# Kernel optimization log

Hardware: AMD Instinct MI355X
Metric: run time of the kernel (lower is better)

The kernel has to match this reference:

```python
import jax, jax.numpy as jnp
import numpy as np

ATOMS_PER_RES = 24  # hard-coded in .view(B, N_l, -1, 24)
NEG_SLOPE = 0.01    # nn.LeakyReLU default


def setup_inputs() -> dict:
    key = jax.random.key(0)
    ks = jax.random.split(key, 10)
    B, N_l, N_p, H, G = 16, 64, 512, 128, 10
    pos_l = jax.random.normal(ks[0], (B, N_l, 3), jnp.float32) * 5.0
    pos_p = jax.random.normal(ks[1], (B, N_p, ATOMS_PER_RES, 3), jnp.float32) * 5.0
    Interact = jax.random.normal(ks[2], (B, N_l, N_p, H), jnp.float32)
    Interact_mask = jax.random.randint(ks[3], (B, N_l, N_p), 0, 2) > 0
    W_pi = jax.random.normal(ks[4], (H, G), jnp.float32) * 0.05
    b_pi = jnp.zeros((G,), jnp.float32)
    W_sigma = jax.random.normal(ks[5], (H, G), jnp.float32) * 0.05
    b_sigma = jnp.zeros((G,), jnp.float32)
    W_mu = jax.random.normal(ks[6], (H, G), jnp.float32) * 0.05
    b_mu = jnp.zeros((G,), jnp.float32)
    return {
        "pos_l": pos_l, "pos_p": pos_p, "Interact": Interact,
        "Interact_mask": Interact_mask,
        "W_pi": W_pi, "b_pi": b_pi,
        "W_sigma": W_sigma, "b_sigma": b_sigma,
        "W_mu": W_mu, "b_mu": b_mu,
    }


def _min_dist(pos_l, pos_p):
    # pos_l: [B, N_l, 3]; pos_p: [B, N_p, 24, 3]
    B, N_l, _ = pos_l.shape
    Y = pos_p.reshape(B, -1, 3)  # [B, N_p*24, 3]
    d2 = (jnp.sum(pos_l * pos_l, axis=-1)[..., None]
          + jnp.sum(Y * Y, axis=-1)[:, None, :]
          - 2.0 * jnp.einsum('bic,bjc->bij', pos_l, Y))  # [B, N_l, N_p*24]
    dist = jnp.nan_to_num(jnp.sqrt(d2), nan=10000.0)
    # min over the 24 atoms of each residue -> [B, N_l, N_p]
    return dist.reshape(B, N_l, -1, ATOMS_PER_RES).min(axis=-1)


def reference(pos_l, pos_p, Interact, Interact_mask,
              W_pi, b_pi, W_sigma, b_sigma, W_mu, b_mu):
    leaky = lambda x: jax.nn.leaky_relu(x, NEG_SLOPE)
    dist = _min_dist(pos_l, pos_p)                       # [B, N_l, N_p]
    # original gathers dist[Interact_mask]; keep static shape, zero-fill masked-out
    dist_masked = jnp.where(Interact_mask, dist, 0.0)
    pi = jax.nn.softmax(Interact @ W_pi + b_pi, axis=-1)          # [B,N_l,N_p,G]
    sigma = jnp.clip(leaky(Interact @ W_sigma + b_sigma) + 1.1, 1e-6, None)
    mu = leaky(Interact @ W_mu + b_mu) + 1.0
    return pi, sigma, mu, dist_masked, Interact_mask
```

## Files before the change

### kernel.cpp

```cpp
#include <hip/hip_runtime.h>
#include <cmath>

#define NB 16
#define NL 64
#define NP 512
#define NH 128
#define NG 10
#define ROWS (NB * NL * NP)

#define OFF_PI    ((size_t)0)
#define OFF_SIGMA ((size_t)5242880)
#define OFF_MU    ((size_t)10485760)
#define OFF_DIST  ((size_t)15728640)
#define OFF_MASK  ((size_t)16252928)

typedef __attribute__((ext_vector_type(8))) short short8;
typedef __attribute__((ext_vector_type(4))) float f32x4;

__device__ __forceinline__ unsigned pk2(float a, float b) {
    unsigned ua = __float_as_uint(a);
    unsigned ub = __float_as_uint(b);
    ua = (ua + 0x7fffu + ((ua >> 16) & 1u)) >> 16;
    ub = (ub + 0x7fffu + ((ub >> 16) & 1u)) & 0xffff0000u;
    return ua | ub;
}

__global__ __launch_bounds__(512) void k_pack(
    const float* __restrict__ Wpi, const float* __restrict__ Wsg,
    const float* __restrict__ Wmu, uint4* __restrict__ tbl)
{
    int e    = threadIdx.x;
    int lane = e & 63;
    int n    = (e >> 6) & 1;
    int ks   = e >> 7;
    int lrow = lane & 15, lkg = lane >> 4;
    int col  = n * 16 + lrow;
    float w[8];
    #pragma unroll
    for (int j = 0; j < 8; ++j) {
        int k = ks * 32 + lkg * 8 + j;
        float v = 0.0f;
        if      (col < 10) v = Wpi[k * NG + col];
        else if (col < 20) v = Wsg[k * NG + col - 10];
        else if (col < 30) v = Wmu[k * NG + col - 20];
        w[j] = v;
    }
    uint4 u = {pk2(w[0], w[1]), pk2(w[2], w[3]),
               pk2(w[4], w[5]), pk2(w[6], w[7])};
    tbl[e] = u;
}

__global__ __launch_bounds__(256, 3) void k_fused(
    const float* __restrict__ pos_l,
    const float* __restrict__ pos_p,
    const int*   __restrict__ mask,
    const float* __restrict__ X,
    const uint4* __restrict__ wtbl,
    const float* __restrict__ bpi,
    const float* __restrict__ bsg,
    const float* __restrict__ bmu,
    float* __restrict__ out_pi,
    float* __restrict__ out_sg,
    float* __restrict__ out_mu,
    float* __restrict__ dist_out,
    float* __restrict__ mask_out)
{
    __shared__ __align__(16) float cs[4 * 64 * 36];

    const int tid  = threadIdx.x;
    const int wv   = tid >> 6;
    const int lane = tid & 63;
    const int lrow = lane & 15;
    const int lkg  = lane >> 4;
    const int idx  = blockIdx.x * 256 + tid;
    const size_t row0 = (size_t)blockIdx.x * 256;

    uint4 bu0[4], bu1[4];
    #pragma unroll
    for (int ks = 0; ks < 4; ++ks) {
        bu0[ks] = wtbl[(ks * 2 + 0) * 64 + lane];
        bu1[ks] = wtbl[(ks * 2 + 1) * 64 + lane];
    }

    const int c0 = lrow, c1 = lrow + 16;
    const float bv0 = (c0 < 10) ? bpi[c0] : bsg[c0 - 10];
    const float bv1 = (c1 < 20) ? bsg[c1 - 10] : (c1 < 30 ? bmu[c1 - 20] : 0.0f);

    const float* xbase = X + (row0 + wv * 64 + lrow) * NH + lkg * 8;
    float4 xc[8], xn[8];
    #pragma unroll
    for (int q = 0; q < 8; ++q)
        xc[q] = *(const float4*)(xbase + (q >> 1) * 32 + (q & 1) * 4);

    {
        int p  = idx & (NP - 1);
        int bl = idx >> 9;
        int b  = bl >> 6;

        const float* xl = pos_l + bl * 3;
        float x0 = xl[0], x1 = xl[1], x2 = xl[2];
        float qs = x0 * x0 + x1 * x1 + x2 * x2;

        const float4* yp = (const float4*)(pos_p + ((size_t)(b * NP + p)) * 72);

        float m2 = 1e30f;
        #pragma unroll
        for (int q = 0; q < 6; ++q) {
            float4 v0 = yp[q * 3 + 0];
            float4 v1 = yp[q * 3 + 1];
            float4 v2 = yp[q * 3 + 2];
            float c[12] = {v0.x, v0.y, v0.z, v0.w,
                           v1.x, v1.y, v1.z, v1.w,
                           v2.x, v2.y, v2.z, v2.w};
            #pragma unroll
            for (int a = 0; a < 4; ++a) {
                float yx = c[a * 3 + 0], yy = c[a * 3 + 1], yz = c[a * 3 + 2];
                float d2 = qs + (yx * yx + yy * yy + yz * yz)
                              - 2.0f * (x0 * yx + x1 * yy + x2 * yz);
                d2 = (d2 >= 0.0f) ? d2 : 1e8f;
                m2 = fminf(m2, d2);
            }
        }
        float m = sqrtf(m2);
        int mk = mask[idx];
        dist_out[idx] = mk ? m : 0.0f;
        mask_out[idx] = mk ? 1.0f : 0.0f;
    }

    f32x4 acc[4][2];
    #pragma unroll
    for (int m = 0; m < 4; ++m) {
        acc[m][0] = (f32x4){bv0, bv0, bv0, bv0};
        acc[m][1] = (f32x4){bv1, bv1, bv1, bv1};
    }

    #pragma unroll
    for (int m = 0; m < 4; ++m) {
        if (m < 3) {
            const float* ap = xbase + (size_t)(m + 1) * 16 * NH;
            #pragma unroll
            for (int q = 0; q < 8; ++q)
                xn[q] = *(const float4*)(ap + (q >> 1) * 32 + (q & 1) * 4);
        }
        #pragma unroll
        for (int ks = 0; ks < 4; ++ks) {
            float4 lo = xc[ks * 2], hi = xc[ks * 2 + 1];
            uint4 ua = {pk2(lo.x, lo.y), pk2(lo.z, lo.w),
                        pk2(hi.x, hi.y), pk2(hi.z, hi.w)};
            short8 af = __builtin_bit_cast(short8, ua);
            acc[m][0] = __builtin_amdgcn_mfma_f32_16x16x32_bf16(
                af, __builtin_bit_cast(short8, bu0[ks]), acc[m][0], 0, 0, 0);
            acc[m][1] = __builtin_amdgcn_mfma_f32_16x16x32_bf16(
                af, __builtin_bit_cast(short8, bu1[ks]), acc[m][1], 0, 0, 0);
        }
        #pragma unroll
        for (int q = 0; q < 8; ++q) xc[q] = xn[q];
    }

    float* cw = cs + wv * (64 * 36);
    #pragma unroll
    for (int m = 0; m < 4; ++m)
        #pragma unroll
        for (int n = 0; n < 2; ++n)
            #pragma unroll
            for (int r = 0; r < 4; ++r)
                cw[(m * 16 + lkg * 4 + r) * 36 + n * 16 + lrow] = acc[m][n][r];

    const float* myrow = cs + wv * (64 * 36) + lane * 36;
    float a[32];
    #pragma unroll
    for (int j = 0; j < 8; ++j)
        *(float4*)&a[4 * j] = *(const float4*)&myrow[4 * j];

    const size_t ro = (size_t)idx * NG;

    float mx = a[0];
    #pragma unroll
    for (int g = 1; g < NG; ++g) mx = fmaxf(mx, a[g]);
    float e[NG], ssum = 0.0f;
    #pragma unroll
    for (int g = 0; g < NG; ++g) { e[g] = __expf(a[g] - mx); ssum += e[g]; }
    float inv = 1.0f / ssum;
    #pragma unroll
    for (int g = 0; g < 5; ++g)
        *(float2*)&out_pi[ro + 2 * g] = make_float2(e[2 * g] * inv,
                                                    e[2 * g + 1] * inv);

    #pragma unroll
    for (int g = 0; g < 5; ++g) {
        float xa = a[10 + 2 * g], xb = a[10 + 2 * g + 1];
        float va = fmaxf((xa >= 0.0f ? xa : 0.01f * xa) + 1.1f, 1e-6f);
        float vb = fmaxf((xb >= 0.0f ? xb : 0.01f * xb) + 1.1f, 1e-6f);
        *(float2*)&out_sg[ro + 2 * g] = make_float2(va, vb);
    }

    #pragma unroll
    for (int g = 0; g < 5; ++g) {
        float xa = a[20 + 2 * g], xb = a[20 + 2 * g + 1];
        float va = (xa >= 0.0f ? xa : 0.01f * xa) + 1.0f;
        float vb = (xb >= 0.0f ? xb : 0.01f * xb) + 1.0f;
        *(float2*)&out_mu[ro + 2 * g] = make_float2(va, vb);
    }
}

extern "C" void kernel_launch(void* const* d_in, const int* in_sizes, int n_in,
                              void* d_out, int out_size, void* d_ws, size_t ws_size,
                              hipStream_t stream) {
    const float* pos_l    = (const float*)d_in[0];
    const float* pos_p    = (const float*)d_in[1];
    const float* Interact = (const float*)d_in[2];
    const int*   mask     = (const int*)  d_in[3];
    const float* Wpi      = (const float*)d_in[4];
    const float* bpi      = (const float*)d_in[5];
    const float* Wsg      = (const float*)d_in[6];
    const float* bsg      = (const float*)d_in[7];
    const float* Wmu      = (const float*)d_in[8];
    const float* bmu      = (const float*)d_in[9];

    float* out      = (float*)d_out;
    float* out_pi   = out + OFF_PI;
    float* out_sg   = out + OFF_SIGMA;
    float* out_mu   = out + OFF_MU;
    float* out_dist = out + OFF_DIST;
    float* out_mask = out + OFF_MASK;

    uint4* wtbl = (uint4*)d_ws;

    hipLaunchKernelGGL(k_pack, dim3(1), dim3(512), 0, stream,
                       Wpi, Wsg, Wmu, wtbl);
    hipLaunchKernelGGL(k_fused, dim3(ROWS / 256), dim3(256), 0, stream,
                       pos_l, pos_p, mask, Interact, wtbl,
                       bpi, bsg, bmu,
                       out_pi, out_sg, out_mu, out_dist, out_mask);
}
```

Measured before the change: 410.9 us.

## Stage Interact tiles and weight table through swizzled LDS with coalesced loads

The X (Interact) matrix is now loaded with a coalesced pattern: each group of 8 lanes reads one contiguous 128-byte row segment per k-slice. The data goes into an XOR-swizzled shared-memory tile, from which the MFMA A-fragments are read, with the next k-slice prefetched into registers while the current one computes. The packed weight table is also placed in LDS instead of being held per-lane in registers, and the epilogue reuses the same buffer. Launch bounds raise the occupancy target from 3 to 4 blocks, at the cost of extra __syncthreads barriers and LDS traffic per k-slice.

New measurement: 458.0 us. 1.11x slower.

```diff
diff --git a/kernel.cpp b/kernel.cpp
--- a/kernel.cpp
+++ b/kernel.cpp
@@ -50,7 +50,7 @@
     tbl[e] = u;
 }
 
-__global__ __launch_bounds__(256, 3) void k_fused(
+__global__ __launch_bounds__(256, 4) void k_fused(
     const float* __restrict__ pos_l,
     const float* __restrict__ pos_p,
     const int*   __restrict__ mask,
@@ -65,7 +65,8 @@
     float* __restrict__ dist_out,
     float* __restrict__ mask_out)
 {
-    __shared__ __align__(16) float cs[4 * 64 * 36];
+    __shared__ __align__(16) float xs[256 * 32];
+    __shared__ __align__(16) uint4 bt[512];
 
     const int tid  = threadIdx.x;
     const int wv   = tid >> 6;
@@ -75,22 +76,22 @@
     const int idx  = blockIdx.x * 256 + tid;
     const size_t row0 = (size_t)blockIdx.x * 256;
 
-    uint4 bu0[4], bu1[4];
-    #pragma unroll
-    for (int ks = 0; ks < 4; ++ks) {
-        bu0[ks] = wtbl[(ks * 2 + 0) * 64 + lane];
-        bu1[ks] = wtbl[(ks * 2 + 1) * 64 + lane];
-    }
+    const int a_ = lane >> 3;
+    const int b_ = lane & 7;
+    const int wchunk = b_ ^ a_;
+    const int wro    = wv * 8 + a_;
+    const float* gsb = X + (row0 + wro) * NH + b_ * 4;
+
+    uint4 bt0 = wtbl[tid];
+    uint4 bt1 = wtbl[tid + 256];
+    float4 pf[8];
+    #pragma unroll
+    for (int j = 0; j < 8; ++j)
+        pf[j] = *(const float4*)(gsb + (size_t)j * 32 * NH);
 
     const int c0 = lrow, c1 = lrow + 16;
     const float bv0 = (c0 < 10) ? bpi[c0] : bsg[c0 - 10];
     const float bv1 = (c1 < 20) ? bsg[c1 - 10] : (c1 < 30 ? bmu[c1 - 20] : 0.0f);
-
-    const float* xbase = X + (row0 + wv * 64 + lrow) * NH + lkg * 8;
-    float4 xc[8], xn[8];
-    #pragma unroll
-    for (int q = 0; q < 8; ++q)
-        xc[q] = *(const float4*)(xbase + (q >> 1) * 32 + (q & 1) * 4);
 
     {
         int p  = idx & (NP - 1);
@@ -127,6 +128,13 @@
         mask_out[idx] = mk ? 1.0f : 0.0f;
     }
 
+    bt[tid]       = bt0;
+    bt[tid + 256] = bt1;
+    #pragma unroll
+    for (int j = 0; j < 8; ++j)
+        *(float4*)&xs[(wro + j * 32) * 32 + wchunk * 4] = pf[j];
+    __syncthreads();
+
     f32x4 acc[4][2];
     #pragma unroll
     for (int m = 0; m < 4; ++m) {
@@ -134,43 +142,55 @@
         acc[m][1] = (f32x4){bv1, bv1, bv1, bv1};
     }
 
-    #pragma unroll
-    for (int m = 0; m < 4; ++m) {
-        if (m < 3) {
-            const float* ap = xbase + (size_t)(m + 1) * 16 * NH;
-            #pragma unroll
-            for (int q = 0; q < 8; ++q)
-                xn[q] = *(const float4*)(ap + (q >> 1) * 32 + (q & 1) * 4);
-        }
+    const int s7 = lrow & 7;
+    #pragma unroll
+    for (int t = 0; t < 4; ++t) {
+        if (t < 3) {
+            #pragma unroll
+            for (int j = 0; j < 8; ++j)
+                pf[j] = *(const float4*)(gsb + (size_t)j * 32 * NH
+                                             + (t + 1) * 32);
+        }
+        short8 bf0 = __builtin_bit_cast(short8, bt[(t * 2 + 0) * 64 + lane]);
+        short8 bf1 = __builtin_bit_cast(short8, bt[(t * 2 + 1) * 64 + lane]);
+
         #pragma unroll
-        for (int ks = 0; ks < 4; ++ks) {
-            float4 lo = xc[ks * 2], hi = xc[ks * 2 + 1];
+        for (int m = 0; m < 4; ++m) {
+            const int R = wv * 64 + m * 16 + lrow;
+            float4 lo = *(const float4*)&xs[R * 32 + ((2 * lkg)     ^ s7) * 4];
+            float4 hi = *(const float4*)&xs[R * 32 + ((2 * lkg + 1) ^ s7) * 4];
             uint4 ua = {pk2(lo.x, lo.y), pk2(lo.z, lo.w),
                         pk2(hi.x, hi.y), pk2(hi.z, hi.w)};
             short8 af = __builtin_bit_cast(short8, ua);
-            acc[m][0] = __builtin_amdgcn_mfma_f32_16x16x32_bf16(
-                af, __builtin_bit_cast(short8, bu0[ks]), acc[m][0], 0, 0, 0);
-            acc[m][1] = __builtin_amdgcn_mfma_f32_16x16x32_bf16(
-                af, __builtin_bit_cast(short8, bu1[ks]), acc[m][1], 0, 0, 0);
-        }
-        #pragma unroll
-        for (int q = 0; q < 8; ++q) xc[q] = xn[q];
-    }
-
-    float* cw = cs + wv * (64 * 36);
+            acc[m][0] = __builtin_amdgcn_mfma_f32_16x16x32_bf16(af, bf0, acc[m][0], 0, 0, 0);
+            acc[m][1] = __builtin_amdgcn_mfma_f32_16x16x32_bf16(af, bf1, acc[m][1], 0, 0, 0);
+        }
+
+        if (t < 3) {
+            __syncthreads();
+            #pragma unroll
+            for (int j = 0; j < 8; ++j)
+                *(float4*)&xs[(wro + j * 32) * 32 + wchunk * 4] = pf[j];
+            __syncthreads();
+        }
+    }
+
     #pragma unroll
     for (int m = 0; m < 4; ++m)
         #pragma unroll
         for (int n = 0; n < 2; ++n)
             #pragma unroll
-            for (int r = 0; r < 4; ++r)
-                cw[(m * 16 + lkg * 4 + r) * 36 + n * 16 + lrow] = acc[m][n][r];
-
-    const float* myrow = cs + wv * (64 * 36) + lane * 36;
+            for (int r = 0; r < 4; ++r) {
+                int Rabs = wv * 64 + m * 16 + lkg * 4 + r;
+                int ch   = n * 4 + (lrow >> 2);
+                xs[Rabs * 32 + ((ch ^ (Rabs & 7)) * 4) + (lrow & 3)]
+                    = acc[m][n][r];
+            }
+
     float a[32];
     #pragma unroll
     for (int j = 0; j < 8; ++j)
-        *(float4*)&a[4 * j] = *(const float4*)&myrow[4 * j];
+        *(float4*)&a[4 * j] = *(const float4*)&xs[tid * 32 + ((j ^ (tid & 7)) * 4)];
 
     const size_t ro = (size_t)idx * NG;
 
```
